# Optimization experiments

Measured on AMD Instinct MI355X. Metric: run time of the kernel, lower is better.

The kernel has to match this reference:

```python
import jax, jax.numpy as jnp
import numpy as np

B, C, H, W = 4, 256, 64, 64
DQ = C // 8

def setup_inputs() -> dict:
    key = jax.random.key(0)
    ks = jax.random.split(key, 7)
    x = jax.random.normal(ks[0], (B, C, H, W), dtype=jnp.float32)
    # 1x1 convs == per-pixel linear layers: weight [out, in], bias [out]
    Wq = jax.random.normal(ks[1], (DQ, C), dtype=jnp.float32) * (1.0 / np.sqrt(C))
    bq = jax.random.normal(ks[2], (DQ,), dtype=jnp.float32) * 0.01
    Wk = jax.random.normal(ks[3], (DQ, C), dtype=jnp.float32) * (1.0 / np.sqrt(C))
    bk = jax.random.normal(ks[4], (DQ,), dtype=jnp.float32) * 0.01
    Wv = jax.random.normal(ks[5], (C, C), dtype=jnp.float32) * (1.0 / np.sqrt(C))
    bv = jax.random.normal(ks[6], (C,), dtype=jnp.float32) * 0.01
    return {"x": x, "Wq": Wq, "bq": bq, "Wk": Wk, "bk": bk, "Wv": Wv, "bv": bv}

def reference(x, Wq, bq, Wk, bk, Wv, bv):
    b, c, h, w = x.shape
    n = h * w
    xf = x.reshape(b, c, n)                                  # [b,c,n]
    Q = jnp.einsum('dc,bcn->bnd', Wq, xf) + bq               # [b,n,dq]
    K = jnp.einsum('dc,bcn->bdn', Wk, xf) + bk[None, :, None]  # [b,dq,n]
    A = jax.nn.softmax(jnp.einsum('bnd,bdm->bnm', Q, K), axis=-1)  # [b,n,n]
    V = jnp.einsum('oc,bcn->bon', Wv, xf) + bv[None, :, None]      # [b,c,n]
    # torch: bmm(V, A^T) -> out[b,c,i] = sum_j V[b,c,j] * A[b,i,j]
    out = jnp.einsum('bcj,bij->bci', V, A)
    return x + out.reshape(b, c, h, w)
```

## Files before the change

### kernel.cpp

```cpp
#include <hip/hip_runtime.h>
#include <math.h>

#define BB 4
#define CC 256
#define NN 4096
#define DQ 32
#define LOG2E 1.44269504f

typedef _Float16 half8 __attribute__((ext_vector_type(8)));
typedef _Float16 half4 __attribute__((ext_vector_type(4)));
typedef float float4v __attribute__((ext_vector_type(4)));

__global__ __launch_bounds__(64) void prep_kernel(
    const float* __restrict__ Wq, const float* __restrict__ bq,
    const float* __restrict__ Wk, const float* __restrict__ bk,
    const float* __restrict__ Wv, const float* __restrict__ bv,
    _Float16* __restrict__ Wh, float* __restrict__ bh)
{
    int o = blockIdx.x, t = threadIdx.x;
    const float* src; float scale = 1.0f, bias;
    if (o < DQ)            { src = Wq + o * CC;        scale = LOG2E; bias = bq[o] * LOG2E; }
    else if (o < 2 * DQ)   { src = Wk + (o - DQ) * CC;                bias = bk[o - DQ]; }
    else                   { src = Wv + (o - 2 * DQ) * CC;            bias = bv[o - 2 * DQ]; }
    float4 v = *(const float4*)(src + t * 4);
    half4 h = { (_Float16)(v.x * scale), (_Float16)(v.y * scale),
                (_Float16)(v.z * scale), (_Float16)(v.w * scale) };
    *(half4*)(Wh + o * CC + t * 4) = h;
    if (t == 0) bh[o] = bias;
}

__global__ __launch_bounds__(256) void proj_kernel(
    const float* __restrict__ x, const _Float16* __restrict__ Wh,
    const float* __restrict__ bh,
    _Float16* __restrict__ Qt, _Float16* __restrict__ Kt,
    _Float16* __restrict__ Vh)
{
    __shared__ _Float16 xl[64 * 256];
    __shared__ _Float16 os_qk[64 * 72];
    __shared__ _Float16 os_v[256 * 72];

    const int tid = threadIdx.x;
    const int lane = tid & 63, w = tid >> 6;
    const int i16 = lane & 15, q = lane >> 4;
    const int n0 = blockIdx.x * 64, b = blockIdx.y;

    const float* xb = x + (size_t)b * CC * NN + n0;
    #pragma unroll
    for (int u = 0; u < 16; ++u) {
        int idx = u * 256 + tid;
        int c = idx >> 4, n4 = idx & 15;
        float4 v = *(const float4*)(xb + (size_t)c * NN + n4 * 4);
        int chunk = c >> 3, cl = c & 7;
        float vv[4] = {v.x, v.y, v.z, v.w};
        #pragma unroll
        for (int e = 0; e < 4; ++e) {
            int n = n4 * 4 + e;
            xl[n * 256 + ((chunk ^ (n & 31)) * 8) + cl] = (_Float16)vv[e];
        }
    }

    float4v acc[5][4];
    const int obase = 80 * w;
    #pragma unroll
    for (int ot = 0; ot < 5; ++ot) {
        float4 b4 = *(const float4*)(bh + obase + 16 * ot + 4 * q);
        #pragma unroll
        for (int nt = 0; nt < 4; ++nt)
            acc[ot][nt] = (float4v){b4.x, b4.y, b4.z, b4.w};
    }
    __syncthreads();

    #pragma unroll
    for (int k = 0; k < 8; ++k) {
        half8 af[5], bf[4];
        #pragma unroll
        for (int ot = 0; ot < 5; ++ot)
            af[ot] = *(const half8*)(Wh + (size_t)(obase + 16 * ot + i16) * CC + k * 32 + 8 * q);
        #pragma unroll
        for (int nt = 0; nt < 4; ++nt) {
            int n = 16 * nt + i16;
            bf[nt] = *(const half8*)&xl[n * 256 + (((4 * k + q) ^ (n & 31)) * 8)];
        }
        #pragma unroll
        for (int ot = 0; ot < 5; ++ot)
            #pragma unroll
            for (int nt = 0; nt < 4; ++nt)
                acc[ot][nt] = __builtin_amdgcn_mfma_f32_16x16x32_f16(af[ot], bf[nt], acc[ot][nt], 0, 0, 0);
    }

    #pragma unroll
    for (int ot = 0; ot < 5; ++ot) {
        int og = obase + 16 * ot;
        #pragma unroll
        for (int nt = 0; nt < 4; ++nt) {
            int n = 16 * nt + i16;
            if (og < 64) {
                half4 hv = { (_Float16)acc[ot][nt][0], (_Float16)acc[ot][nt][1],
                             (_Float16)acc[ot][nt][2], (_Float16)acc[ot][nt][3] };
                *(half4*)&os_qk[n * 72 + og + 4 * q] = hv;
            } else {
                int cb = og - 64 + 4 * q;
                #pragma unroll
                for (int r = 0; r < 4; ++r)
                    os_v[(cb + r) * 72 + n] = (_Float16)acc[ot][nt][r];
            }
        }
    }
    __syncthreads();

    _Float16* Qtb = Qt + (size_t)b * NN * DQ;
    _Float16* Ktb = Kt + (size_t)b * NN * DQ;
    #pragma unroll
    for (int u = 0; u < 2; ++u) {
        int ct = u * 256 + tid;
        int n = ct >> 3, p = ct & 7;
        half8 hv = *(const half8*)&os_qk[n * 72 + 8 * p];
        if (p < 4) *(half8*)(Qtb + (size_t)(n0 + n) * DQ + 8 * p) = hv;
        else       *(half8*)(Ktb + (size_t)(n0 + n) * DQ + 8 * (p - 4)) = hv;
    }
    _Float16* Vb = Vh + (size_t)b * CC * NN;
    #pragma unroll
    for (int u = 0; u < 8; ++u) {
        int c = u * 32 + (tid >> 3), p = tid & 7;
        half8 hv = *(const half8*)&os_v[c * 72 + 8 * p];
        *(half8*)(Vb + (size_t)c * NN + n0 + 8 * p) = hv;
    }
}

__global__ __launch_bounds__(256) void rowstat_kernel(
    const _Float16* __restrict__ Qt, const _Float16* __restrict__ Kt,
    float* __restrict__ M2, float* __restrict__ L)
{
    __shared__ _Float16 k_lds[64 * 32];
    const int tid = threadIdx.x;
    const int lane = tid & 63, w = tid >> 6;
    const int i16 = lane & 15, q = lane >> 4;
    const int q0 = blockIdx.x * 64, js = blockIdx.y, b = blockIdx.z;

    const _Float16* Qtb = Qt + (size_t)b * NN * DQ;
    const _Float16* Ktb = Kt + (size_t)b * NN * DQ;
    half8 qb = *(const half8*)(Qtb + (size_t)(q0 + 16 * w + i16) * DQ + 8 * q);

    float m = -INFINITY, l = 0.f;
    for (int j0 = js * 2048; j0 < (js + 1) * 2048; j0 += 64) {
        __syncthreads();
        {
            int j = tid >> 2, dg = tid & 3;
            half8 kv = *(const half8*)(Ktb + (size_t)(j0 + j) * DQ + 8 * dg);
            *(half8*)&k_lds[j * 32 + ((dg ^ (j & 3)) * 8)] = kv;
        }
        __syncthreads();
        float4v s[4];
        #pragma unroll
        for (int jt = 0; jt < 4; ++jt) {
            int j = 16 * jt + i16;
            half8 ka = *(const half8*)&k_lds[j * 32 + ((q ^ (j & 3)) * 8)];
            float4v z = {0.f, 0.f, 0.f, 0.f};
            s[jt] = __builtin_amdgcn_mfma_f32_16x16x32_f16(ka, qb, z, 0, 0, 0);
        }
        float tmax = s[0][0];
        #pragma unroll
        for (int jt = 0; jt < 4; ++jt)
            #pragma unroll
            for (int r = 0; r < 4; ++r)
                tmax = fmaxf(tmax, s[jt][r]);
        float mnew = fmaxf(m, tmax);
        float sum = 0.f;
        #pragma unroll
        for (int jt = 0; jt < 4; ++jt)
            #pragma unroll
            for (int r = 0; r < 4; ++r)
                sum += exp2f(s[jt][r] - mnew);
        l = l * exp2f(m - mnew) + sum;
        m = mnew;
    }
    #pragma unroll
    for (int off = 16; off <= 32; off <<= 1) {
        float mo = __shfl_xor(m, off, 64);
        float lo = __shfl_xor(l, off, 64);
        float mn = fmaxf(m, mo);
        l = l * exp2f(m - mn) + lo * exp2f(mo - mn);
        m = mn;
    }
    if (q == 0) {
        int qi = q0 + 16 * w + i16;
        M2[((size_t)b * 2 + js) * NN + qi] = m;
        L[((size_t)b * 2 + js) * NN + qi] = l;
    }
}

__global__ __launch_bounds__(256) void attn_kernel(
    const float* __restrict__ x,
    const _Float16* __restrict__ Qt, const _Float16* __restrict__ Kt,
    const _Float16* __restrict__ Vh,
    const float* __restrict__ M2, const float* __restrict__ L,
    float* __restrict__ out)
{
    __shared__ _Float16 k_lds[64 * 32];
    __shared__ _Float16 v_lds[256 * 64];
    __shared__ _Float16 ps[32 * 72];

    const int tid = threadIdx.x;
    const int w = tid >> 6, lane = tid & 63;
    const int i16 = lane & 15, q = lane >> 4;
    const int i0 = blockIdx.x * 32, b = blockIdx.y;

    const _Float16* Ktb = Kt + (size_t)b * NN * DQ;
    const _Float16* Vb  = Vh + (size_t)b * CC * NN;

    float m2v[2], linv[2];
    #pragma unroll
    for (int it = 0; it < 2; ++it) {
        int qi = i0 + 16 * it + i16;
        float m0 = M2[((size_t)b * 2 + 0) * NN + qi];
        float m1 = M2[((size_t)b * 2 + 1) * NN + qi];
        float l0 = L[((size_t)b * 2 + 0) * NN + qi];
        float l1 = L[((size_t)b * 2 + 1) * NN + qi];
        float mm = fmaxf(m0, m1);
        float ll = l0 * exp2f(m0 - mm) + l1 * exp2f(m1 - mm);
        m2v[it] = mm;
        linv[it] = 1.0f / ll;
    }

    half8 qb[2];
    {
        const _Float16* Qtb = Qt + (size_t)b * NN * DQ;
        qb[0] = *(const half8*)(Qtb + (size_t)(i0 + i16) * DQ + 8 * q);
        qb[1] = *(const half8*)(Qtb + (size_t)(i0 + 16 + i16) * DQ + 8 * q);
    }

    float4v O[4][2];
    #pragma unroll
    for (int ct = 0; ct < 4; ++ct)
        #pragma unroll
        for (int it = 0; it < 2; ++it)
            O[ct][it] = (float4v){0.f, 0.f, 0.f, 0.f};

    for (int j0 = 0; j0 < NN; j0 += 64) {
        __syncthreads();
        {
            int j = tid >> 2, dg = tid & 3;
            half8 kv = *(const half8*)(Ktb + (size_t)(j0 + j) * DQ + 8 * dg);
            *(half8*)&k_lds[j * 32 + ((dg ^ (j & 3)) * 8)] = kv;
        }
        {
            int cb = tid >> 3, jg = tid & 7;
            #pragma unroll
            for (int u = 0; u < 8; ++u) {
                int c = u * 32 + cb;
                half8 vv = *(const half8*)(Vb + (size_t)c * NN + j0 + jg * 8);
                *(half8*)&v_lds[c * 64 + ((jg ^ (c & 7)) * 8)] = vv;
            }
        }
        __syncthreads();

        {
            int j = 16 * w + i16;
            half8 ka = *(const half8*)&k_lds[j * 32 + ((q ^ (j & 3)) * 8)];
            #pragma unroll
            for (int it = 0; it < 2; ++it) {
                float4v z = {0.f, 0.f, 0.f, 0.f};
                float4v s = __builtin_amdgcn_mfma_f32_16x16x32_f16(ka, qb[it], z, 0, 0, 0);
                half4 hv = { (_Float16)exp2f(s[0] - m2v[it]),
                             (_Float16)exp2f(s[1] - m2v[it]),
                             (_Float16)exp2f(s[2] - m2v[it]),
                             (_Float16)exp2f(s[3] - m2v[it]) };
                *(half4*)&ps[(16 * it + i16) * 72 + 16 * w + 4 * q] = hv;
            }
        }
        __syncthreads();

        half8 pb[2][2];
        #pragma unroll
        for (int ks = 0; ks < 2; ++ks)
            #pragma unroll
            for (int it = 0; it < 2; ++it)
                pb[ks][it] = *(const half8*)&ps[(16 * it + i16) * 72 + 32 * ks + 8 * q];
        #pragma unroll
        for (int ct = 0; ct < 4; ++ct) {
            int c = 64 * w + 16 * ct + i16;
            #pragma unroll
            for (int ks = 0; ks < 2; ++ks) {
                int g = 4 * ks + q;
                half8 va = *(const half8*)&v_lds[c * 64 + ((g ^ (c & 7)) * 8)];
                #pragma unroll
                for (int it = 0; it < 2; ++it)
                    O[ct][it] = __builtin_amdgcn_mfma_f32_16x16x32_f16(va, pb[ks][it], O[ct][it], 0, 0, 0);
            }
        }
    }

    const float* xb = x + (size_t)b * CC * NN;
    float* ob = out + (size_t)b * CC * NN;
    #pragma unroll
    for (int ct = 0; ct < 4; ++ct)
        #pragma unroll
        for (int it = 0; it < 2; ++it)
            #pragma unroll
            for (int r = 0; r < 4; ++r) {
                int c = 64 * w + 16 * ct + 4 * q + r;
                size_t idx = (size_t)c * NN + i0 + 16 * it + i16;
                ob[idx] = xb[idx] + O[ct][it][r] * linv[it];
            }
}

extern "C" void kernel_launch(void* const* d_in, const int* in_sizes, int n_in,
                              void* d_out, int out_size, void* d_ws, size_t ws_size,
                              hipStream_t stream) {
    const float* x  = (const float*)d_in[0];
    const float* Wq = (const float*)d_in[1];
    const float* bq = (const float*)d_in[2];
    const float* Wk = (const float*)d_in[3];
    const float* bk = (const float*)d_in[4];
    const float* Wv = (const float*)d_in[5];
    const float* bv = (const float*)d_in[6];
    float* out = (float*)d_out;

    char* ws = (char*)d_ws;
    _Float16* Wh = (_Float16*)(ws);
    float*    bh = (float*)(ws + 163840);
    _Float16* Qt = (_Float16*)(ws + 262144);
    _Float16* Kt = (_Float16*)(ws + 1310720);
    _Float16* Vh = (_Float16*)(ws + 2359296);
    float*    M2 = (float*)(ws + 10747904);
    float*    L  = (float*)(ws + 10878976);

    prep_kernel<<<dim3(320), 64, 0, stream>>>(Wq, bq, Wk, bk, Wv, bv, Wh, bh);
    proj_kernel<<<dim3(NN / 64, BB), 256, 0, stream>>>(x, Wh, bh, Qt, Kt, Vh);
    rowstat_kernel<<<dim3(NN / 64, 2, BB), 256, 0, stream>>>(Qt, Kt, M2, L);
    attn_kernel<<<dim3(NN / 32, BB), 256, 0, stream>>>(x, Qt, Kt, Vh, M2, L, out);
}
```

Baseline: 205.1 us.

## Drop max-subtraction softmax, stream K/V from global, double-buffer P, retile projection

Removes the running-max tracking from the row-statistics pass and computes only the exp2 sum. The attention kernel folds log2 of that sum into the exponent, so normalization happens inside exp2 and the final rescale disappears. K and V tiles are no longer staged in LDS; they are read directly from global memory/cache per MFMA, with a 128-wide J tile and a double-buffered P buffer that halves the barriers per tile. The projection kernel uses 32-column tiles for more blocks, and the attention grid is remapped to interleave batches. Skipping the max subtraction risks fp32 overflow or fp16 underflow for inputs with large logits, and direct global V loads depend on cache hits.

```diff
diff --git a/kernel.cpp b/kernel.cpp
--- a/kernel.cpp
+++ b/kernel.cpp
@@ -6,6 +6,8 @@
 #define NN 4096
 #define DQ 32
 #define LOG2E 1.44269504f
+#define TJ 128
+#define PS_STRIDE 136
 
 typedef _Float16 half8 __attribute__((ext_vector_type(8)));
 typedef _Float16 half4 __attribute__((ext_vector_type(4)));
@@ -35,56 +37,62 @@
     _Float16* __restrict__ Qt, _Float16* __restrict__ Kt,
     _Float16* __restrict__ Vh)
 {
-    __shared__ _Float16 xl[64 * 256];
-    __shared__ _Float16 os_qk[64 * 72];
-    __shared__ _Float16 os_v[256 * 72];
+    __shared__ _Float16 xl[32 * 256];
+    __shared__ _Float16 os_qk[32 * 72];
+    __shared__ _Float16 os_v[256 * 40];
 
     const int tid = threadIdx.x;
     const int lane = tid & 63, w = tid >> 6;
     const int i16 = lane & 15, q = lane >> 4;
-    const int n0 = blockIdx.x * 64, b = blockIdx.y;
+    const int n0 = blockIdx.x * 32, b = blockIdx.y;
 
     const float* xb = x + (size_t)b * CC * NN + n0;
     #pragma unroll
-    for (int u = 0; u < 16; ++u) {
-        int idx = u * 256 + tid;
-        int c = idx >> 4, n4 = idx & 15;
-        float4 v = *(const float4*)(xb + (size_t)c * NN + n4 * 4);
-        int chunk = c >> 3, cl = c & 7;
-        float vv[4] = {v.x, v.y, v.z, v.w};
+    for (int u = 0; u < 2; ++u) {
+        int c0 = 4 * (tid >> 3) + 128 * u;
+        int nn = 4 * (tid & 7);
+        float4 rr[4];
+        #pragma unroll
+        for (int j = 0; j < 4; ++j)
+            rr[j] = *(const float4*)(xb + (size_t)(c0 + j) * NN + nn);
         #pragma unroll
         for (int e = 0; e < 4; ++e) {
-            int n = n4 * 4 + e;
-            xl[n * 256 + ((chunk ^ (n & 31)) * 8) + cl] = (_Float16)vv[e];
-        }
-    }
-
-    float4v acc[5][4];
+            int n = nn + e;
+            half4 h = { (_Float16)((const float*)&rr[0])[e],
+                        (_Float16)((const float*)&rr[1])[e],
+                        (_Float16)((const float*)&rr[2])[e],
+                        (_Float16)((const float*)&rr[3])[e] };
+            int chunk = (c0 >> 3) ^ (n & 31);
+            *(half4*)&xl[n * 256 + chunk * 8 + (c0 & 7)] = h;
+        }
+    }
+
+    float4v acc[5][2];
     const int obase = 80 * w;
     #pragma unroll
     for (int ot = 0; ot < 5; ++ot) {
         float4 b4 = *(const float4*)(bh + obase + 16 * ot + 4 * q);
         #pragma unroll
-        for (int nt = 0; nt < 4; ++nt)
+        for (int nt = 0; nt < 2; ++nt)
             acc[ot][nt] = (float4v){b4.x, b4.y, b4.z, b4.w};
     }
     __syncthreads();
 
     #pragma unroll
     for (int k = 0; k < 8; ++k) {
-        half8 af[5], bf[4];
+        half8 af[5], bf[2];
         #pragma unroll
         for (int ot = 0; ot < 5; ++ot)
             af[ot] = *(const half8*)(Wh + (size_t)(obase + 16 * ot + i16) * CC + k * 32 + 8 * q);
         #pragma unroll
-        for (int nt = 0; nt < 4; ++nt) {
+        for (int nt = 0; nt < 2; ++nt) {
             int n = 16 * nt + i16;
             bf[nt] = *(const half8*)&xl[n * 256 + (((4 * k + q) ^ (n & 31)) * 8)];
         }
         #pragma unroll
         for (int ot = 0; ot < 5; ++ot)
             #pragma unroll
-            for (int nt = 0; nt < 4; ++nt)
+            for (int nt = 0; nt < 2; ++nt)
                 acc[ot][nt] = __builtin_amdgcn_mfma_f32_16x16x32_f16(af[ot], bf[nt], acc[ot][nt], 0, 0, 0);
     }
 
@@ -92,7 +100,7 @@
     for (int ot = 0; ot < 5; ++ot) {
         int og = obase + 16 * ot;
         #pragma unroll
-        for (int nt = 0; nt < 4; ++nt) {
+        for (int nt = 0; nt < 2; ++nt) {
             int n = 16 * nt + i16;
             if (og < 64) {
                 half4 hv = { (_Float16)acc[ot][nt][0], (_Float16)acc[ot][nt][1],
@@ -102,7 +110,7 @@
                 int cb = og - 64 + 4 * q;
                 #pragma unroll
                 for (int r = 0; r < 4; ++r)
-                    os_v[(cb + r) * 72 + n] = (_Float16)acc[ot][nt][r];
+                    os_v[(cb + r) * 40 + n] = (_Float16)acc[ot][nt][r];
             }
         }
     }
@@ -110,28 +118,25 @@
 
     _Float16* Qtb = Qt + (size_t)b * NN * DQ;
     _Float16* Ktb = Kt + (size_t)b * NN * DQ;
-    #pragma unroll
-    for (int u = 0; u < 2; ++u) {
-        int ct = u * 256 + tid;
-        int n = ct >> 3, p = ct & 7;
+    {
+        int n = tid >> 3, p = tid & 7;
         half8 hv = *(const half8*)&os_qk[n * 72 + 8 * p];
         if (p < 4) *(half8*)(Qtb + (size_t)(n0 + n) * DQ + 8 * p) = hv;
         else       *(half8*)(Ktb + (size_t)(n0 + n) * DQ + 8 * (p - 4)) = hv;
     }
     _Float16* Vb = Vh + (size_t)b * CC * NN;
     #pragma unroll
-    for (int u = 0; u < 8; ++u) {
-        int c = u * 32 + (tid >> 3), p = tid & 7;
-        half8 hv = *(const half8*)&os_v[c * 72 + 8 * p];
+    for (int u = 0; u < 4; ++u) {
+        int c = u * 64 + (tid >> 2), p = tid & 3;
+        half8 hv = *(const half8*)&os_v[c * 40 + 8 * p];
         *(half8*)(Vb + (size_t)c * NN + n0 + 8 * p) = hv;
     }
 }
 
 __global__ __launch_bounds__(256) void rowstat_kernel(
     const _Float16* __restrict__ Qt, const _Float16* __restrict__ Kt,
-    float* __restrict__ M2, float* __restrict__ L)
-{
-    __shared__ _Float16 k_lds[64 * 32];
+    float* __restrict__ L)
+{
     const int tid = threadIdx.x;
     const int lane = tid & 63, w = tid >> 6;
     const int i16 = lane & 15, q = lane >> 4;
@@ -141,85 +146,53 @@
     const _Float16* Ktb = Kt + (size_t)b * NN * DQ;
     half8 qb = *(const half8*)(Qtb + (size_t)(q0 + 16 * w + i16) * DQ + 8 * q);
 
-    float m = -INFINITY, l = 0.f;
-    for (int j0 = js * 2048; j0 < (js + 1) * 2048; j0 += 64) {
-        __syncthreads();
-        {
-            int j = tid >> 2, dg = tid & 3;
-            half8 kv = *(const half8*)(Ktb + (size_t)(j0 + j) * DQ + 8 * dg);
-            *(half8*)&k_lds[j * 32 + ((dg ^ (j & 3)) * 8)] = kv;
-        }
-        __syncthreads();
+    float l = 0.f;
+    #pragma unroll 2
+    for (int j0 = js * (NN / 2); j0 < (js + 1) * (NN / 2); j0 += 64) {
         float4v s[4];
         #pragma unroll
         for (int jt = 0; jt < 4; ++jt) {
-            int j = 16 * jt + i16;
-            half8 ka = *(const half8*)&k_lds[j * 32 + ((q ^ (j & 3)) * 8)];
+            half8 ka = *(const half8*)(Ktb + (size_t)(j0 + 16 * jt + i16) * DQ + 8 * q);
             float4v z = {0.f, 0.f, 0.f, 0.f};
             s[jt] = __builtin_amdgcn_mfma_f32_16x16x32_f16(ka, qb, z, 0, 0, 0);
         }
-        float tmax = s[0][0];
         #pragma unroll
         for (int jt = 0; jt < 4; ++jt)
             #pragma unroll
             for (int r = 0; r < 4; ++r)
-                tmax = fmaxf(tmax, s[jt][r]);
-        float mnew = fmaxf(m, tmax);
-        float sum = 0.f;
-        #pragma unroll
-        for (int jt = 0; jt < 4; ++jt)
-            #pragma unroll
-            for (int r = 0; r < 4; ++r)
-                sum += exp2f(s[jt][r] - mnew);
-        l = l * exp2f(m - mnew) + sum;
-        m = mnew;
-    }
-    #pragma unroll
-    for (int off = 16; off <= 32; off <<= 1) {
-        float mo = __shfl_xor(m, off, 64);
-        float lo = __shfl_xor(l, off, 64);
-        float mn = fmaxf(m, mo);
-        l = l * exp2f(m - mn) + lo * exp2f(mo - mn);
-        m = mn;
-    }
-    if (q == 0) {
-        int qi = q0 + 16 * w + i16;
-        M2[((size_t)b * 2 + js) * NN + qi] = m;
-        L[((size_t)b * 2 + js) * NN + qi] = l;
-    }
+                l += exp2f(s[jt][r]);
+    }
+    l += __shfl_xor(l, 16, 64);
+    l += __shfl_xor(l, 32, 64);
+    if (q == 0)
+        L[((size_t)b * 2 + js) * NN + q0 + 16 * w + i16] = l;
 }
 
 __global__ __launch_bounds__(256) void attn_kernel(
     const float* __restrict__ x,
     const _Float16* __restrict__ Qt, const _Float16* __restrict__ Kt,
-    const _Float16* __restrict__ Vh,
-    const float* __restrict__ M2, const float* __restrict__ L,
+    const _Float16* __restrict__ Vh, const float* __restrict__ L,
     float* __restrict__ out)
 {
-    __shared__ _Float16 k_lds[64 * 32];
-    __shared__ _Float16 v_lds[256 * 64];
-    __shared__ _Float16 ps[32 * 72];
+    __shared__ _Float16 ps[2][32 * PS_STRIDE];
 
     const int tid = threadIdx.x;
     const int w = tid >> 6, lane = tid & 63;
     const int i16 = lane & 15, q = lane >> 4;
-    const int i0 = blockIdx.x * 32, b = blockIdx.y;
+    const int id = blockIdx.x;
+    const int b = (id & 7) >> 1;
+    const int i0 = 32 * ((id >> 3) + 64 * (id & 1));
 
     const _Float16* Ktb = Kt + (size_t)b * NN * DQ;
     const _Float16* Vb  = Vh + (size_t)b * CC * NN;
 
-    float m2v[2], linv[2];
+    float lg[2];
     #pragma unroll
     for (int it = 0; it < 2; ++it) {
         int qi = i0 + 16 * it + i16;
-        float m0 = M2[((size_t)b * 2 + 0) * NN + qi];
-        float m1 = M2[((size_t)b * 2 + 1) * NN + qi];
         float l0 = L[((size_t)b * 2 + 0) * NN + qi];
         float l1 = L[((size_t)b * 2 + 1) * NN + qi];
-        float mm = fmaxf(m0, m1);
-        float ll = l0 * exp2f(m0 - mm) + l1 * exp2f(m1 - mm);
-        m2v[it] = mm;
-        linv[it] = 1.0f / ll;
+        lg[it] = log2f(l0 + l1);
     }
 
     half8 qb[2];
@@ -236,53 +209,40 @@
         for (int it = 0; it < 2; ++it)
             O[ct][it] = (float4v){0.f, 0.f, 0.f, 0.f};
 
-    for (int j0 = 0; j0 < NN; j0 += 64) {
-        __syncthreads();
-        {
-            int j = tid >> 2, dg = tid & 3;
-            half8 kv = *(const half8*)(Ktb + (size_t)(j0 + j) * DQ + 8 * dg);
-            *(half8*)&k_lds[j * 32 + ((dg ^ (j & 3)) * 8)] = kv;
-        }
-        {
-            int cb = tid >> 3, jg = tid & 7;
-            #pragma unroll
-            for (int u = 0; u < 8; ++u) {
-                int c = u * 32 + cb;
-                half8 vv = *(const half8*)(Vb + (size_t)c * NN + j0 + jg * 8);
-                *(half8*)&v_lds[c * 64 + ((jg ^ (c & 7)) * 8)] = vv;
-            }
-        }
-        __syncthreads();
-
-        {
-            int j = 16 * w + i16;
-            half8 ka = *(const half8*)&k_lds[j * 32 + ((q ^ (j & 3)) * 8)];
+    for (int t = 0; t < NN / TJ; ++t) {
+        const int j0 = t * TJ;
+        _Float16* psb = &ps[t & 1][0];
+
+        #pragma unroll
+        for (int st = 0; st < 2; ++st) {
+            int j = j0 + 32 * w + 16 * st + i16;
+            half8 ka = *(const half8*)(Ktb + (size_t)j * DQ + 8 * q);
             #pragma unroll
             for (int it = 0; it < 2; ++it) {
                 float4v z = {0.f, 0.f, 0.f, 0.f};
                 float4v s = __builtin_amdgcn_mfma_f32_16x16x32_f16(ka, qb[it], z, 0, 0, 0);
-                half4 hv = { (_Float16)exp2f(s[0] - m2v[it]),
-                             (_Float16)exp2f(s[1] - m2v[it]),
-                             (_Float16)exp2f(s[2] - m2v[it]),
-                             (_Float16)exp2f(s[3] - m2v[it]) };
-                *(half4*)&ps[(16 * it + i16) * 72 + 16 * w + 4 * q] = hv;
+                half4 hv = { (_Float16)exp2f(s[0] - lg[it]),
+                             (_Float16)exp2f(s[1] - lg[it]),
+                             (_Float16)exp2f(s[2] - lg[it]),
+                             (_Float16)exp2f(s[3] - lg[it]) };
+                *(half4*)&psb[(16 * it + i16) * PS_STRIDE + 32 * w + 16 * st + 4 * q] = hv;
             }
         }
         __syncthreads();
 
-        half8 pb[2][2];
-        #pragma unroll
-        for (int ks = 0; ks < 2; ++ks)
+        half8 pb[4][2];
+        #pragma unroll
+        for (int ks = 0; ks < 4; ++ks)
             #pragma unroll
             for (int it = 0; it < 2; ++it)
-                pb[ks][it] = *(const half8*)&ps[(16 * it + i16) * 72 + 32 * ks + 8 * q];
+                pb[ks][it] = *(const half8*)&psb[(16 * it + i16) * PS_STRIDE + 32 * ks + 8 * q];
         #pragma unroll
         for (int ct = 0; ct < 4; ++ct) {
             int c = 64 * w + 16 * ct + i16;
-            #pragma unroll
-            for (int ks = 0; ks < 2; ++ks) {
-                int g = 4 * ks + q;
-                half8 va = *(const half8*)&v_lds[c * 64 + ((g ^ (c & 7)) * 8)];
+            const _Float16* vrow = Vb + (size_t)c * NN + j0;
+            #pragma unroll
+            for (int ks = 0; ks < 4; ++ks) {
+                half8 va = *(const half8*)(vrow + 32 * ks + 8 * q);
                 #pragma unroll
                 for (int it = 0; it < 2; ++it)
                     O[ct][it] = __builtin_amdgcn_mfma_f32_16x16x32_f16(va, pb[ks][it], O[ct][it], 0, 0, 0);
@@ -300,7 +260,7 @@
             for (int r = 0; r < 4; ++r) {
                 int c = 64 * w + 16 * ct + 4 * q + r;
                 size_t idx = (size_t)c * NN + i0 + 16 * it + i16;
-                ob[idx] = xb[idx] + O[ct][it][r] * linv[it];
+                ob[idx] = xb[idx] + O[ct][it][r];
             }
 }
 
@@ -322,11 +282,10 @@
     _Float16* Qt = (_Float16*)(ws + 262144);
     _Float16* Kt = (_Float16*)(ws + 1310720);
     _Float16* Vh = (_Float16*)(ws + 2359296);
-    float*    M2 = (float*)(ws + 10747904);
-    float*    L  = (float*)(ws + 10878976);
+    float*    L  = (float*)(ws + 10747904);
 
     prep_kernel<<<dim3(320), 64, 0, stream>>>(Wq, bq, Wk, bk, Wv, bv, Wh, bh);
-    proj_kernel<<<dim3(NN / 64, BB), 256, 0, stream>>>(x, Wh, bh, Qt, Kt, Vh);
-    rowstat_kernel<<<dim3(NN / 64, 2, BB), 256, 0, stream>>>(Qt, Kt, M2, L);
-    attn_kernel<<<dim3(NN / 32, BB), 256, 0, stream>>>(x, Qt, Kt, Vh, M2, L, out);
-}
+    proj_kernel<<<dim3(NN / 32, BB), 256, 0, stream>>>(x, Wh, bh, Qt, Kt, Vh);
+    rowstat_kernel<<<dim3(NN / 64, 2, BB), 256, 0, stream>>>(Qt, Kt, L);
+    attn_kernel<<<dim3(512), 256, 0, stream>>>(x, Qt, Kt, Vh, L, out);
+}
```

New measurement: 265.3 us. 29.4% more time.
